# Performance work log

Hardware: AMD Instinct MI355X
Metric: run time of the kernel (lower is better)

The kernel has to match this reference:

```python
import jax, jax.numpy as jnp
import numpy as np

D_MODEL = 1024
EXPAND = 2
HEADDIM = 64
D_STATE = 64
CHUNK = 64
D_INNER = EXPAND * D_MODEL          # 2048
NHEADS = D_INNER // HEADDIM         # 32
D_MLP = int(2.5 * D_MODEL)          # 2560
BATCH = 2
SEQLEN = 4096
PROJ = 2 * D_INNER + 2 * NHEADS * D_STATE + NHEADS + NHEADS * (D_STATE // 2)


def rmsnorm(x, w, eps=1e-5):
    return x * jax.lax.rsqrt(jnp.mean(x * x, axis=-1, keepdims=True) + eps) * w


def apply_rope(x, angles):
    x1 = x[..., 0::2]
    x2 = x[..., 1::2]
    c = jnp.cos(angles)
    s = jnp.sin(angles)
    ev = c * x1 - s * x2
    od = s * x1 + c * x2
    return jnp.stack([ev, od], axis=-1).reshape(x.shape)


def segsum(x):
    # x: (b,h,c,l) -> (b,h,c,l,l); [i,j] = sum_{j<k<=i} x_k (no -inf mask, as in source)
    T = x.shape[-1]
    xx = jnp.broadcast_to(x[..., :, None], x.shape + (T,))
    mask = jnp.tril(jnp.ones((T, T), dtype=bool), -1)
    xx = jnp.where(mask, xx, 0.0)
    return jnp.cumsum(xx, axis=-2)


def ssd(x, A, B, C, chunk):
    # x: (b,s,h,p), A: (b,s,h), B/C: (b,s,h,n); s % chunk == 0
    b, s, h, p = x.shape
    n = B.shape[-1]
    c = s // chunk
    x_c = x.reshape(b, c, chunk, h, p).transpose(0, 1, 3, 2, 4)  # (b,c,h,l,p)
    B_c = B.reshape(b, c, chunk, h, n).transpose(0, 1, 3, 2, 4)  # (b,c,h,l,n)
    C_c = C.reshape(b, c, chunk, h, n).transpose(0, 1, 3, 2, 4)
    A_c = A.reshape(b, c, chunk, h).transpose(0, 1, 3, 2)        # (b,c,h,l)
    A_cum = jnp.cumsum(A_c, axis=-1)
    L = jnp.exp(segsum(A_c.transpose(0, 2, 1, 3))).transpose(0, 2, 1, 3, 4)  # (b,c,h,l,l)
    Bx = jnp.einsum('bchln,bchlp->bchpn', B_c, x_c)
    Y_diag = jnp.einsum('bchln,bchls,bchpn->bchlp', C_c, L, Bx)
    decay_states = jnp.exp(A_cum[..., -1:] - A_cum)
    states = jnp.einsum('bchln,bchl,bchlp->bchpn', B_c, decay_states, x_c)  # (b,c,h,p,n)
    decay_chunk = jnp.exp(A_cum[..., -1])  # (b,c,h)
    h0 = jnp.zeros_like(states[:, 0])

    def step(carry, inp):
        dec, st = inp  # dec: (b,h), st: (b,h,p,n)
        carry = carry * dec[:, :, None, None] + st
        return carry, carry

    _, hs = jax.lax.scan(step, h0, (decay_chunk.transpose(1, 0, 2),
                                    states.transpose(1, 0, 2, 3, 4)))
    final_states = hs.transpose(1, 0, 2, 3, 4)  # (b,c,h,p,n)
    Y_off = jnp.einsum('bchln,bchpn,bchl->bchlp', C_c, final_states, jnp.exp(A_cum))
    Y = (Y_diag + Y_off).transpose(0, 1, 3, 2, 4).reshape(b, s, h * p)
    return Y


def setup_inputs() -> dict:
    key = jax.random.key(0)
    ks = jax.random.split(key, 12)
    sc = 0.02
    return {
        'x': jax.random.normal(ks[0], (BATCH, SEQLEN, D_MODEL), jnp.float32),
        'norm1_w': jnp.ones((D_MODEL,), jnp.float32),
        'norm2_w': jnp.ones((D_MODEL,), jnp.float32),
        'W_in': sc * jax.random.normal(ks[1], (D_MODEL, PROJ), jnp.float32),
        'W_out': sc * jax.random.normal(ks[2], (D_INNER, D_MODEL), jnp.float32),
        'A_log': jax.random.uniform(ks[3], (NHEADS,), jnp.float32, -4.0, -1.0),
        'D_param': jnp.ones((NHEADS,), jnp.float32),
        'dt_bias': jax.random.uniform(ks[4], (NHEADS,), jnp.float32, 0.001, 0.1),
        'B_bias': jnp.ones((1, NHEADS, D_STATE), jnp.float32),
        'C_bias': jnp.ones((1, NHEADS, D_STATE), jnp.float32),
        'Bn_w': jnp.ones((D_STATE,), jnp.float32),
        'Cn_w': jnp.ones((D_STATE,), jnp.float32),
        'Wg': sc * jax.random.normal(ks[5], (D_MODEL, D_MLP), jnp.float32),
        'Wu': sc * jax.random.normal(ks[6], (D_MODEL, D_MLP), jnp.float32),
        'Wd': sc * jax.random.normal(ks[7], (D_MLP, D_MODEL), jnp.float32),
    }


def reference(x, norm1_w, norm2_w, W_in, W_out, A_log, D_param, dt_bias,
              B_bias, C_bias, Bn_w, Cn_w, Wg, Wu, Wd):
    b, s, _ = x.shape
    h = rmsnorm(x, norm1_w)
    proj = h @ W_in
    i = 0
    z = proj[..., i:i + D_INNER]; i += D_INNER
    x_ssm = proj[..., i:i + D_INNER]; i += D_INNER
    B = proj[..., i:i + NHEADS * D_STATE].reshape(b, s, NHEADS, D_STATE); i += NHEADS * D_STATE
    C = proj[..., i:i + NHEADS * D_STATE].reshape(b, s, NHEADS, D_STATE); i += NHEADS * D_STATE
    dt = proj[..., i:i + NHEADS]; i += NHEADS
    theta = proj[..., i:].reshape(b, s, NHEADS, D_STATE // 2)
    dt = jax.nn.softplus(dt + dt_bias)                 # (b,s,h)
    A = -jnp.exp(A_log) * dt
    alpha = jnp.exp(A)
    gamma = (alpha - 1.0) / (A + 1e-6) * 0.5 + 1.0
    B = rmsnorm(B, Bn_w) + B_bias
    C = rmsnorm(C, Cn_w) + C_bias
    cum_theta = jnp.cumsum(dt[..., None] * theta, axis=1)
    B = apply_rope(B, cum_theta)
    C = apply_rope(C, cum_theta)
    x_ssm = x_ssm.reshape(b, s, NHEADS, HEADDIM)
    y = ssd(x_ssm * gamma[..., None], A, B, C, CHUNK)
    skip = jnp.broadcast_to((D_param * x_ssm.sum(-1))[..., None], x_ssm.shape)
    y = y + skip.reshape(b, s, -1)
    y = y * (z * jax.nn.sigmoid(z))
    y = y @ W_out
    x = x + y
    h2 = rmsnorm(x, norm2_w)
    g = h2 @ Wg
    x = x + ((g * jax.nn.sigmoid(g)) * (h2 @ Wu)) @ Wd
    return x
```

## Files before the change

kernel.cpp:

```cpp
#include <hip/hip_runtime.h>
#include <cstdint>
#include <cmath>


typedef __bf16 bf16;
typedef __bf16 bf16x2 __attribute__((ext_vector_type(2)));
typedef __bf16 bf16x4 __attribute__((ext_vector_type(4)));
typedef __bf16 bf16x8 __attribute__((ext_vector_type(8)));
typedef float fx4 __attribute__((ext_vector_type(4)));

#define DEV __device__ __forceinline__

#define OFF_PROJ    0ull
#define OFF_HHI     134217728ull
#define OFF_HLO     150994944ull
#define OFF_WTIN    167772160ull
#define OFF_WTHI    184549376ull
#define OFF_WTLO    186908672ull
#define OFF_PROJT   189267968ull
#define OFF_BX      189267968ull
#define OFF_STATES  222822400ull
#define OFF_WTOUT   222822400ull
#define OFF_WTGU    227016704ull
#define OFF_WTD     237502464ull
#define OFF_ABUF    256376832ull
#define OFF_XSUM    257425408ull
#define OFF_ROWSUM  258473984ull
#define OFF_EXPA    260571136ull
#define OFF_DCHUNK  262668288ull
#define OFF_GAMMA   262684672ull
#define WS_NEEDED   263733248ull

#define OFF_GU      0ull
#define OFF_MBF     83886080ull

DEV void async_copy16(void* lds, const void* gptr) {
  __builtin_amdgcn_global_load_lds(
      (const __attribute__((address_space(1))) unsigned int*)(gptr),
      (__attribute__((address_space(3))) unsigned int*)(lds),
      16, 0, 0);
}

DEV float warp_sum64(float v) {
  #pragma unroll
  for (int o = 32; o; o >>= 1) v += __shfl_xor(v, o);
  return v;
}

DEV float red16(float v) {
  v += __shfl_xor(v, 1); v += __shfl_xor(v, 2);
  v += __shfl_xor(v, 4); v += __shfl_xor(v, 8);
  return v;
}

DEV float softplus_f(float x) { return x > 20.f ? x : log1pf(expf(x)); }
DEV float sigmoid_f(float x) { return 1.f / (1.f + expf(-x)); }

__global__ __launch_bounds__(256) void transpose_cast(
    const float* __restrict__ src, int ld, int col0,
    bf16* __restrict__ dst, int R, int C)
{
  __shared__ float tile[32][33];
  const int c0 = blockIdx.x * 32, r0 = blockIdx.y * 32;
  const int tx = threadIdx.x & 31, ty = threadIdx.x >> 5;
  #pragma unroll
  for (int ii = 0; ii < 4; ++ii) {
    int i = ty + ii * 8;
    int c = c0 + tx;
    tile[i][tx] = (c < C) ? src[(size_t)(r0 + i) * ld + col0 + c] : 0.f;
  }
  __syncthreads();
  #pragma unroll
  for (int ii = 0; ii < 4; ++ii) {
    int i = ty + ii * 8;
    dst[(size_t)(c0 + i) * R + r0 + tx] = (bf16)tile[tx][i];
  }
}

__global__ __launch_bounds__(256) void transpose_cast_hilo(
    const float* __restrict__ src, int ld, int col0,
    bf16* __restrict__ dhi, bf16* __restrict__ dlo, int R, int C)
{
  __shared__ float tile[32][33];
  const int c0 = blockIdx.x * 32, r0 = blockIdx.y * 32;
  const int tx = threadIdx.x & 31, ty = threadIdx.x >> 5;
  #pragma unroll
  for (int ii = 0; ii < 4; ++ii) {
    int i = ty + ii * 8;
    int c = c0 + tx;
    tile[i][tx] = (c < C) ? src[(size_t)(r0 + i) * ld + col0 + c] : 0.f;
  }
  __syncthreads();
  #pragma unroll
  for (int ii = 0; ii < 4; ++ii) {
    int i = ty + ii * 8;
    float v = tile[tx][i];
    bf16 hi = (bf16)v;
    size_t o = (size_t)(c0 + i) * R + r0 + tx;
    dhi[o] = hi;
    dlo[o] = (bf16)(v - (float)hi);
  }
}

__global__ __launch_bounds__(256) void rmsnorm_kernel(
    const float* __restrict__ x, const float* __restrict__ w,
    bf16* __restrict__ hi, bf16* __restrict__ lo)
{
  __shared__ float red[4];
  const size_t row = blockIdx.x;
  const int tid = threadIdx.x;
  float4 v = ((const float4*)(x + row * 1024))[tid];
  float ss = v.x * v.x + v.y * v.y + v.z * v.z + v.w * v.w;
  ss = warp_sum64(ss);
  if ((tid & 63) == 0) red[tid >> 6] = ss;
  __syncthreads();
  float tot = red[0] + red[1] + red[2] + red[3];
  float s = rsqrtf(tot * (1.f / 1024.f) + 1e-5f);
  float4 wv = ((const float4*)w)[tid];
  float h0 = v.x * s * wv.x, h1 = v.y * s * wv.y, h2 = v.z * s * wv.z, h3 = v.w * s * wv.w;
  bf16x4 hv = { (bf16)h0, (bf16)h1, (bf16)h2, (bf16)h3 };
  *(bf16x4*)(hi + row * 1024 + tid * 4) = hv;
  if (lo) {
    bf16x4 lv = { (bf16)(h0 - (float)hv[0]), (bf16)(h1 - (float)hv[1]),
                  (bf16)(h2 - (float)hv[2]), (bf16)(h3 - (float)hv[3]) };
    *(bf16x4*)(lo + row * 1024 + tid * 4) = lv;
  }
}

__global__ __launch_bounds__(256) void gemm_tail(
    const bf16* Ahi, const bf16* Alo, const bf16* Whi, const bf16* Wlo,
    float* Cout)
{
  __shared__ bf16 Ah[128 * 64], Al[128 * 64], Bh[128 * 64], Bl[128 * 64];
  const int tid = threadIdx.x, wid = tid >> 6, lane = tid & 63;
  const int m0 = blockIdx.y * 128, n0 = blockIdx.x * 128;
  const int wm = (wid & 1) * 64, wn = (wid >> 1) * 64;
  fx4 acc[4][4];
  #pragma unroll
  for (int i = 0; i < 4; ++i)
    #pragma unroll
    for (int j = 0; j < 4; ++j) { fx4 z = {0.f, 0.f, 0.f, 0.f}; acc[i][j] = z; }

  const int srow = wid * 32 + (lane >> 3);
  const int slot = lane & 7;

  for (int k0 = 0; k0 < 1024; k0 += 64) {
    __syncthreads();
    #pragma unroll
    for (int i = 0; i < 4; ++i) {
      int m = srow + i * 8;
      int cA = ((slot ^ (m & 7)) * 8);
      size_t ao = (size_t)(m0 + m) * 1024 + k0 + cA;
      async_copy16(&Ah[wid * 2048 + i * 512], Ahi + ao);
      async_copy16(&Al[wid * 2048 + i * 512], Alo + ao);
      int n = srow + i * 8;
      int cB = ((slot ^ (n & 7)) * 8);
      size_t bo = (size_t)(n0 + n) * 1024 + k0 + cB;
      async_copy16(&Bh[wid * 2048 + i * 512], Whi + bo);
      async_copy16(&Bl[wid * 2048 + i * 512], Wlo + bo);
    }
    __syncthreads();
    #pragma unroll
    for (int kk = 0; kk < 2; ++kk) {
      bf16x8 ah[4], al[4], bh[4], bl[4];
      #pragma unroll
      for (int i = 0; i < 4; ++i) {
        int mm = wm + i * 16 + (lane & 15);
        int sA = (kk * 4 + (lane >> 4)) ^ (mm & 7);
        ah[i] = *(const bf16x8*)&Ah[mm * 64 + sA * 8];
        al[i] = *(const bf16x8*)&Al[mm * 64 + sA * 8];
        int nn = wn + i * 16 + (lane & 15);
        int sB = (kk * 4 + (lane >> 4)) ^ (nn & 7);
        bh[i] = *(const bf16x8*)&Bh[nn * 64 + sB * 8];
        bl[i] = *(const bf16x8*)&Bl[nn * 64 + sB * 8];
      }
      #pragma unroll
      for (int i = 0; i < 4; ++i)
        #pragma unroll
        for (int j = 0; j < 4; ++j) {
          acc[i][j] = __builtin_amdgcn_mfma_f32_16x16x32_bf16(ah[i], bh[j], acc[i][j], 0, 0, 0);
          acc[i][j] = __builtin_amdgcn_mfma_f32_16x16x32_bf16(ah[i], bl[j], acc[i][j], 0, 0, 0);
          acc[i][j] = __builtin_amdgcn_mfma_f32_16x16x32_bf16(al[i], bh[j], acc[i][j], 0, 0, 0);
        }
    }
  }
  const int r0 = (lane >> 4) * 4, cc = lane & 15;
  #pragma unroll
  for (int i = 0; i < 4; ++i)
    #pragma unroll
    for (int j = 0; j < 4; ++j)
      #pragma unroll
      for (int r = 0; r < 4; ++r) {
        int m = m0 + wm + i * 16 + r0 + r;
        int n = n0 + wn + j * 16 + cc;
        Cout[(size_t)m * 1152 + n] = acc[i][j][r];
      }
}

__global__ __launch_bounds__(256) void dt_kernel(
    float* projT, const float* __restrict__ A_log, const float* __restrict__ dt_bias,
    float* __restrict__ a_buf, float* __restrict__ gamma_buf)
{
  const int idx = blockIdx.x * 256 + threadIdx.x;
  const int t = idx >> 5, h = idx & 31;
  float dtr = projT[(size_t)t * 1152 + h] + dt_bias[h];
  float dt = softplus_f(dtr);
  float a = -expf(A_log[h]) * dt;
  float alpha = expf(a);
  float gamma = (alpha - 1.f) / (a + 1e-6f) * 0.5f + 1.f;
  projT[(size_t)t * 1152 + h] = dt;
  a_buf[idx] = a;
  gamma_buf[idx] = gamma;
}

__global__ __launch_bounds__(512, 2) void gemm_proj256(
    const bf16* __restrict__ A, const bf16* __restrict__ B, bf16* __restrict__ Cout,
    const float* __restrict__ gamma_buf, float* __restrict__ xsum,
    const float* __restrict__ Bn_w, const float* __restrict__ Cn_w,
    const float* __restrict__ B_bias, const float* __restrict__ C_bias)
{
  __shared__ bf16 lds[65536];
  const int tid = threadIdx.x, wid = tid >> 6, lane = tid & 63;
  const int bid = blockIdx.x;
  const int swz = (bid & 7) * 128 + (bid >> 3);
  const int by = swz >> 5, bx = swz & 31;
  const int m0 = by * 256, n0 = bx * 256;
  const int wr = wid >> 2, wc = wid & 3;
  const int fl = lane & 15, fq = lane >> 4;
  const int rloc = wid * 8 + (lane >> 3);
  const int colSwz = ((lane & 7) ^ (lane >> 3)) * 8;

  fx4 acc[8][4];
  #pragma unroll
  for (int i = 0; i < 8; ++i)
    #pragma unroll
    for (int j = 0; j < 4; ++j) { fx4 z = {0.f, 0.f, 0.f, 0.f}; acc[i][j] = z; }

  const bf16* gA = A + (size_t)(m0 + rloc) * 1024 + colSwz;
  const bf16* gB = B + (size_t)(n0 + rloc) * 1024 + colSwz;

  auto STAGE = [&](int u, int h) {
    const bf16* s = (h < 2) ? gB : gA;
    s += (size_t)(h & 1) * 128 * 1024 + u * 64;
    bf16* d = &lds[((u & 1) * 4 + h) * 8192 + wid * 512];
    async_copy16(d, s);
    async_copy16(d + 4096, s + 64 * 1024);
  };

  STAGE(0, 0); STAGE(0, 1); STAGE(0, 2); STAGE(0, 3);
  STAGE(1, 0); STAGE(1, 1);
  asm volatile("s_waitcnt vmcnt(4)" ::: "memory");
  __builtin_amdgcn_s_barrier();

  const int NT = 16;
  bf16x8 bfrag[4][2];
  for (int t = 0; t < NT; ++t) {
    const int Bb = (t & 1) * 32768;
    const int Ab = Bb + 16384;
    #pragma unroll
    for (int p = 0; p < 4; ++p) {
      bf16x8 af[2][2];
      if (p == 0) {
        #pragma unroll
        for (int j = 0; j < 4; ++j) {
          int nn = wc * 64 + j * 16 + fl;
          #pragma unroll
          for (int kk = 0; kk < 2; ++kk) {
            int q = (kk * 4 + fq) ^ (nn & 7);
            bfrag[j][kk] = *(const bf16x8*)&lds[Bb + nn * 64 + q * 8];
          }
        }
      }
      #pragma unroll
      for (int ii = 0; ii < 2; ++ii) {
        int mm = wr * 128 + (p * 2 + ii) * 16 + fl;
        #pragma unroll
        for (int kk = 0; kk < 2; ++kk) {
          int q = (kk * 4 + fq) ^ (mm & 7);
          af[ii][kk] = *(const bf16x8*)&lds[Ab + mm * 64 + q * 8];
        }
      }
      {
        int H = 4 * t + 6 + p;
        if (H < 4 * NT) STAGE(H >> 2, H & 3);
      }
      if (p == 3) asm volatile("s_waitcnt vmcnt(4)" ::: "memory");
      __builtin_amdgcn_s_barrier();
      asm volatile("s_waitcnt lgkmcnt(0)" ::: "memory");
      __builtin_amdgcn_sched_barrier(0);
      __builtin_amdgcn_s_setprio(1);
      #pragma unroll
      for (int ii = 0; ii < 2; ++ii)
        #pragma unroll
        for (int j = 0; j < 4; ++j)
          #pragma unroll
          for (int kk = 0; kk < 2; ++kk)
            acc[p * 2 + ii][j] = __builtin_amdgcn_mfma_f32_16x16x32_bf16(
                af[ii][kk], bfrag[j][kk], acc[p * 2 + ii][j], 0, 0, 0);
      __builtin_amdgcn_s_setprio(0);
      __builtin_amdgcn_s_barrier();
    }
  }

  const int reg = bx >> 3;
  const int hh = ((n0 + wc * 64) & 2047) >> 6;
  const int mwb = m0 + wr * 128;
  const int nwb = n0 + wc * 64;
  if (reg == 0) {
    #pragma unroll
    for (int i = 0; i < 8; ++i)
      #pragma unroll
      for (int j = 0; j < 4; ++j)
        #pragma unroll
        for (int r = 0; r < 4; ++r) {
          int m = mwb + i * 16 + fq * 4 + r;
          int n = nwb + j * 16 + fl;
          Cout[(size_t)m * 8192 + n] = (bf16)acc[i][j][r];
        }
  } else if (reg == 1) {
    #pragma unroll
    for (int i = 0; i < 8; ++i)
      #pragma unroll
      for (int r = 0; r < 4; ++r) {
        float s = acc[i][0][r] + acc[i][1][r] + acc[i][2][r] + acc[i][3][r];
        s = red16(s);
        int m = mwb + i * 16 + fq * 4 + r;
        if (fl == 0) xsum[(size_t)m * 32 + hh] = s;
        float g = gamma_buf[(size_t)m * 32 + hh];
        #pragma unroll
        for (int j = 0; j < 4; ++j) {
          int n = nwb + j * 16 + fl;
          Cout[(size_t)m * 8192 + n] = (bf16)(acc[i][j][r] * g);
        }
      }
  } else {
    const float* w = (reg == 2) ? Bn_w : Cn_w;
    const float* bias = (reg == 2) ? B_bias : C_bias;
    #pragma unroll
    for (int i = 0; i < 8; ++i)
      #pragma unroll
      for (int r = 0; r < 4; ++r) {
        float ss = acc[i][0][r] * acc[i][0][r] + acc[i][1][r] * acc[i][1][r]
                 + acc[i][2][r] * acc[i][2][r] + acc[i][3][r] * acc[i][3][r];
        ss = red16(ss);
        float sc = rsqrtf(ss * (1.f / 64.f) + 1e-5f);
        int m = mwb + i * 16 + fq * 4 + r;
        #pragma unroll
        for (int j = 0; j < 4; ++j) {
          int c = j * 16 + fl;
          Cout[(size_t)m * 8192 + nwb + c] =
              (bf16)(acc[i][j][r] * sc * w[c] + bias[hh * 64 + c]);
        }
      }
  }
}

template <int MODE>
__global__ __launch_bounds__(512, 2) void gemm128x256(
    const bf16* __restrict__ A, const bf16* __restrict__ B, void* __restrict__ Cout,
    const float* __restrict__ resid, int NT, int lda, int ldc, int nbx)
{
  __shared__ bf16 lds[49152];
  const int tid = threadIdx.x, wid = tid >> 6, lane = tid & 63;
  const int cpx = gridDim.x >> 3;
  const int bid = blockIdx.x;
  const int swz = (bid & 7) * cpx + (bid >> 3);
  const int by = swz / nbx, bx = swz - by * nbx;
  const int m0 = by * 128, n0 = bx * 256;
  const int wr = wid >> 2, wc = wid & 3;
  const int fl = lane & 15, fq = lane >> 4;
  const int rloc = wid * 8 + (lane >> 3);
  const int colSwz = ((lane & 7) ^ (lane >> 3)) * 8;
  const int K = NT * 64;

  fx4 acc[4][4];
  #pragma unroll
  for (int i = 0; i < 4; ++i)
    #pragma unroll
    for (int j = 0; j < 4; ++j) { fx4 z = {0.f, 0.f, 0.f, 0.f}; acc[i][j] = z; }

  const bf16* gA = A + (size_t)(m0 + rloc) * lda + colSwz;
  const bf16* gB = B + (size_t)(n0 + rloc) * K + colSwz;

  auto STAGE = [&](int u, int h) {
    const bf16* s;
    size_t str;
    if (h < 2) { s = gB + (size_t)h * 128 * K; str = (size_t)K; }
    else       { s = gA;                       str = (size_t)lda; }
    s += u * 64;
    bf16* d = &lds[((u & 1) * 3 + h) * 8192 + wid * 512];
    async_copy16(d, s);
    async_copy16(d + 4096, s + 64 * str);
  };

  STAGE(0, 0); STAGE(0, 1); STAGE(0, 2);
  STAGE(1, 0); STAGE(1, 1);
  asm volatile("s_waitcnt vmcnt(4)" ::: "memory");
  __builtin_amdgcn_s_barrier();

  bf16x8 bfrag[4][2];
  for (int t = 0; t < NT; ++t) {
    const int base = (t & 1) * 24576;
    #pragma unroll
    for (int p = 0; p < 4; ++p) {
      bf16x8 af[2];
      if (p == 0) {
        #pragma unroll
        for (int j = 0; j < 4; ++j) {
          int nn = wc * 64 + j * 16 + fl;
          #pragma unroll
          for (int kk = 0; kk < 2; ++kk) {
            int q = (kk * 4 + fq) ^ (nn & 7);
            bfrag[j][kk] = *(const bf16x8*)&lds[base + (nn >> 7) * 8192 + (nn & 127) * 64 + q * 8];
          }
        }
      }
      {
        int mm = wr * 64 + p * 16 + fl;
        #pragma unroll
        for (int kk = 0; kk < 2; ++kk) {
          int q = (kk * 4 + fq) ^ (mm & 7);
          af[kk] = *(const bf16x8*)&lds[base + 2 * 8192 + mm * 64 + q * 8];
        }
      }
      if (p == 0)      { if (t + 1 < NT) STAGE(t + 1, 2); }
      else if (p == 1) { if (t + 2 < NT) STAGE(t + 2, 0); }
      else if (p == 2) { if (t + 2 < NT) STAGE(t + 2, 1); }
      if (p == 3) asm volatile("s_waitcnt vmcnt(4)" ::: "memory");
      __builtin_amdgcn_s_barrier();
      asm volatile("s_waitcnt lgkmcnt(0)" ::: "memory");
      __builtin_amdgcn_sched_barrier(0);
      __builtin_amdgcn_s_setprio(1);
      #pragma unroll
      for (int j = 0; j < 4; ++j)
        #pragma unroll
        for (int kk = 0; kk < 2; ++kk)
          acc[p][j] = __builtin_amdgcn_mfma_f32_16x16x32_bf16(
              af[kk], bfrag[j][kk], acc[p][j], 0, 0, 0);
      __builtin_amdgcn_s_setprio(0);
      __builtin_amdgcn_s_barrier();
    }
  }

  const int mwb = m0 + wr * 64;
  const int nwb = n0 + wc * 64;
  #pragma unroll
  for (int i = 0; i < 4; ++i)
    #pragma unroll
    for (int j = 0; j < 4; ++j)
      #pragma unroll
      for (int r = 0; r < 4; ++r) {
        int m = mwb + i * 16 + fq * 4 + r;
        int n = nwb + j * 16 + fl;
        size_t off = (size_t)m * ldc + n;
        float v = acc[i][j][r];
        if (MODE == 1) ((bf16*)Cout)[off] = (bf16)v;
        else ((float*)Cout)[off] = v + resid[off];
      }
}

__global__ __launch_bounds__(256) void chunk_sum_kernel(
    const float* __restrict__ projT, float* __restrict__ S)
{
  __shared__ float lds[8 * 288];
  const int blk = blockIdx.x;
  const int hq = blockIdx.y;
  const size_t row0 = (size_t)blk * 64;
  const int tid = threadIdx.x;
  float s = 0.f;
  #pragma unroll 1
  for (int batch = 0; batch < 8; ++batch) {
    __syncthreads();
    const float* src = projT + (row0 + batch * 8) * 1152;
    #pragma unroll
    for (int i = 0; i < 9; ++i) {
      int idx = i * 256 + tid;
      int r = idx / 288, col = idx - r * 288;
      int gcol = (col < 32) ? col : (32 + hq * 256 + (col - 32));
      lds[idx] = src[r * 1152 + gcol];
    }
    __syncthreads();
    int hl = tid >> 5, d = tid & 31;
    #pragma unroll
    for (int r = 0; r < 8; ++r)
      s += lds[r * 288 + hq * 8 + hl] * lds[r * 288 + 32 + hl * 32 + d];
  }
  S[(size_t)blk * 1024 + hq * 256 + tid] = s;
}

__global__ __launch_bounds__(256) void rope_kernel(
    bf16* proj, const float* __restrict__ projT, const float* __restrict__ S)
{
  __shared__ float angs[64 * 33], angc[64 * 33];
  const int blk = blockIdx.x;
  const int b = blk >> 11, c = (blk >> 5) & 63, h = blk & 31;
  const size_t t0 = (size_t)b * 4096 + c * 64;
  const int w = threadIdx.x >> 6, lane = threadIdx.x & 63;
  const float* tr = projT + (t0 + lane) * 1152;
  float dtv = tr[h];
  const float* thp = tr + 32 + h * 32 + w * 8;
  float4 th0 = *(const float4*)thp;
  float4 th1 = *(const float4*)(thp + 4);
  const float* Sp = S + (size_t)(b * 64 + lane) * 1024 + h * 32 + w * 8;
  float4 S0 = *(const float4*)Sp;
  float4 S1 = *(const float4*)(Sp + 4);
  float th[8] = { th0.x, th0.y, th0.z, th0.w, th1.x, th1.y, th1.z, th1.w };
  float Sv[8] = { S0.x, S0.y, S0.z, S0.w, S1.x, S1.y, S1.z, S1.w };
  #pragma unroll 1
  for (int j = 0; j < 8; ++j) {
    int d = w * 8 + j;
    float sv = (lane < c) ? Sv[j] : 0.f;
    float off = warp_sum64(sv);
    float v = dtv * th[j];
    #pragma unroll
    for (int o = 1; o < 64; o <<= 1) { float u = __shfl_up(v, o); if (lane >= o) v += u; }
    float ang = off + v;
    float sn, cs;
    sincosf(ang, &sn, &cs);
    angs[lane * 33 + d] = sn;
    angc[lane * 33 + d] = cs;
  }
  __syncthreads();
  const int tt = threadIdx.x >> 2, q = threadIdx.x & 3;
  const size_t base = (t0 + tt) * 8192 + 4096 + h * 64 + q * 16;
  #pragma unroll
  for (int m = 0; m < 2; ++m) {
    bf16* p = proj + base + m * 2048;
    bf16x8 v0 = *(const bf16x8*)(p);
    bf16x8 v1 = *(const bf16x8*)(p + 8);
    bf16x8 r0, r1;
    #pragma unroll
    for (int pp = 0; pp < 4; ++pp) {
      int d = q * 8 + pp;
      float e1 = (float)v0[2 * pp], e2 = (float)v0[2 * pp + 1];
      float sn = angs[tt * 33 + d], cs = angc[tt * 33 + d];
      r0[2 * pp]     = (bf16)(cs * e1 - sn * e2);
      r0[2 * pp + 1] = (bf16)(sn * e1 + cs * e2);
    }
    #pragma unroll
    for (int pp = 0; pp < 4; ++pp) {
      int d = q * 8 + 4 + pp;
      float e1 = (float)v1[2 * pp], e2 = (float)v1[2 * pp + 1];
      float sn = angs[tt * 33 + d], cs = angc[tt * 33 + d];
      r1[2 * pp]     = (bf16)(cs * e1 - sn * e2);
      r1[2 * pp + 1] = (bf16)(sn * e1 + cs * e2);
    }
    *(bf16x8*)(p) = r0;
    *(bf16x8*)(p + 8) = r1;
  }
}

__global__ __launch_bounds__(256) void ssd1_kernel(
    const bf16* __restrict__ proj, const float* __restrict__ a_buf,
    bf16* __restrict__ Bx, bf16* __restrict__ states,
    float* __restrict__ rowsum, float* __restrict__ expac, float* __restrict__ dchunk)
{
  __shared__ bf16 Xs[64 * 72], Bs[64 * 72];
  __shared__ float acum[64], dsv[64];
  const int blk = blockIdx.x;
  const int h = blk & 31;
  const size_t bs0 = ((size_t)(blk >> 5)) * 64;
  const int tid = threadIdx.x;
  const int l = tid >> 2, p0 = (tid & 3) * 16;
  {
    const bf16* xrow = proj + (bs0 + l) * 8192 + 2048 + h * 64 + p0;
    *(bf16x8*)&Xs[l * 72 + p0]     = ((const bf16x8*)xrow)[0];
    *(bf16x8*)&Xs[l * 72 + p0 + 8] = ((const bf16x8*)xrow)[1];
    const bf16* brow = proj + (bs0 + l) * 8192 + 4096 + h * 64 + p0;
    *(bf16x8*)&Bs[l * 72 + p0]     = ((const bf16x8*)brow)[0];
    *(bf16x8*)&Bs[l * 72 + p0 + 8] = ((const bf16x8*)brow)[1];
  }
  if (tid < 64) {
    float v = a_buf[(bs0 + tid) * 32 + h];
    #pragma unroll
    for (int o = 1; o < 64; o <<= 1) { float u = __shfl_up(v, o); if (tid >= o) v += u; }
    acum[tid] = v;
    float a63 = __shfl(v, 63);
    dsv[tid] = expf(a63 - v);
    expac[(size_t)blk * 64 + tid] = expf(v);
    if (tid == 63) dchunk[blk] = expf(v);
  }
  __syncthreads();
  {
    float al = acum[l];
    float rs = 0.f;
    for (int s = tid & 3; s <= l; s += 4) rs += expf(al - acum[s]);
    rs += __shfl_xor(rs, 1);
    rs += __shfl_xor(rs, 2);
    if ((tid & 3) == 0) rowsum[(size_t)blk * 64 + l] = rs + (float)(63 - l);
  }
  const int wv = tid >> 6, lane = tid & 63;
  const int mi = lane & 15, kq = lane >> 4;
  const int m0 = wv * 16;
  fx4 accB[4], accS[4];
  #pragma unroll
  for (int j4 = 0; j4 < 4; ++j4) { fx4 z = {0.f,0.f,0.f,0.f}; accB[j4] = z; accS[j4] = z; }
  #pragma unroll
  for (int kk = 0; kk < 2; ++kk) {
    const int lb = kk * 32 + kq * 8;
    bf16x8 aX, aXd;
    #pragma unroll
    for (int j = 0; j < 8; ++j) {
      bf16 xv = Xs[(lb + j) * 72 + m0 + mi];
      aX[j] = xv;
      aXd[j] = (bf16)((float)xv * dsv[lb + j]);
    }
    #pragma unroll
    for (int j4 = 0; j4 < 4; ++j4) {
      bf16x8 bB;
      #pragma unroll
      for (int j = 0; j < 8; ++j) bB[j] = Bs[(lb + j) * 72 + j4 * 16 + mi];
      accB[j4] = __builtin_amdgcn_mfma_f32_16x16x32_bf16(aX, bB, accB[j4], 0, 0, 0);
      accS[j4] = __builtin_amdgcn_mfma_f32_16x16x32_bf16(aXd, bB, accS[j4], 0, 0, 0);
    }
  }
  const size_t obase = (size_t)blk * 4096;
  #pragma unroll
  for (int j4 = 0; j4 < 4; ++j4) {
    #pragma unroll
    for (int r = 0; r < 4; ++r) {
      int p = m0 + kq * 4 + r;
      int n = j4 * 16 + mi;
      Bx[obase + p * 64 + n] = (bf16)accB[j4][r];
      states[obase + p * 64 + n] = (bf16)accS[j4][r];
    }
  }
}

__global__ __launch_bounds__(128) void ssd2_kernel(
    bf16* __restrict__ states, const float* __restrict__ dchunk)
{
  const int blk = blockIdx.x;
  const int b = blk >> 9, rest = blk & 511;
  const int h = rest >> 4, q = rest & 15;
  const int e0 = q * 256 + threadIdx.x * 2;
  float fs0 = 0.f, fs1 = 0.f;
  #pragma unroll 2
  for (int c = 0; c < 64; ++c) {
    size_t idx = ((size_t)(b * 2048 + c * 32 + h) * 4096) + e0;
    float dec = dchunk[b * 2048 + c * 32 + h];
    bf16x2 st = *(const bf16x2*)(states + idx);
    fs0 = fs0 * dec + (float)st[0];
    fs1 = fs1 * dec + (float)st[1];
    bf16x2 o = { (bf16)fs0, (bf16)fs1 };
    *(bf16x2*)(states + idx) = o;
  }
}

__global__ __launch_bounds__(256) void ssd3_kernel(
    bf16* proj, const bf16* __restrict__ Bx, const bf16* __restrict__ FS,
    const float* __restrict__ rowsum, const float* __restrict__ expac,
    const float* __restrict__ xsum, const float* __restrict__ D_param)
{
  __shared__ bf16 Cs[64 * 72], BxS[64 * 72], FSs[64 * 72];
  __shared__ float rs_s[64], ea_s[64], sk_s[64];
  const int blk = blockIdx.x;
  const int h = blk & 31;
  const size_t bs0 = ((size_t)(blk >> 5)) * 64;
  const int tid = threadIdx.x;
  const int l = tid >> 2, q0 = (tid & 3) * 16;
  {
    const bf16* crow = proj + (bs0 + l) * 8192 + 6144 + h * 64 + q0;
    *(bf16x8*)&Cs[l * 72 + q0]     = ((const bf16x8*)crow)[0];
    *(bf16x8*)&Cs[l * 72 + q0 + 8] = ((const bf16x8*)crow)[1];
    size_t mb = (size_t)blk * 4096 + l * 64 + q0;
    *(bf16x8*)&BxS[l * 72 + q0]     = ((const bf16x8*)(Bx + mb))[0];
    *(bf16x8*)&BxS[l * 72 + q0 + 8] = ((const bf16x8*)(Bx + mb))[1];
    *(bf16x8*)&FSs[l * 72 + q0]     = ((const bf16x8*)(FS + mb))[0];
    *(bf16x8*)&FSs[l * 72 + q0 + 8] = ((const bf16x8*)(FS + mb))[1];
  }
  if (tid < 64) {
    rs_s[tid] = rowsum[(size_t)blk * 64 + tid];
    ea_s[tid] = expac[(size_t)blk * 64 + tid];
    sk_s[tid] = D_param[h] * xsum[(bs0 + tid) * 32 + h];
  }
  __syncthreads();
  const int wv = tid >> 6, lane = tid & 63;
  const int mi = lane & 15, kq = lane >> 4;
  const int m0 = wv * 16;
  fx4 acc1[4], acc2[4];
  #pragma unroll
  for (int j4 = 0; j4 < 4; ++j4) { fx4 z = {0.f,0.f,0.f,0.f}; acc1[j4] = z; acc2[j4] = z; }
  #pragma unroll
  for (int kk = 0; kk < 2; ++kk) {
    bf16x8 aC = *(const bf16x8*)&Cs[(m0 + mi) * 72 + kk * 32 + kq * 8];
    #pragma unroll
    for (int j4 = 0; j4 < 4; ++j4) {
      bf16x8 bx = *(const bf16x8*)&BxS[(j4 * 16 + mi) * 72 + kk * 32 + kq * 8];
      bf16x8 fs = *(const bf16x8*)&FSs[(j4 * 16 + mi) * 72 + kk * 32 + kq * 8];
      acc1[j4] = __builtin_amdgcn_mfma_f32_16x16x32_bf16(aC, bx, acc1[j4], 0, 0, 0);
      acc2[j4] = __builtin_amdgcn_mfma_f32_16x16x32_bf16(aC, fs, acc2[j4], 0, 0, 0);
    }
  }
  #pragma unroll
  for (int j4 = 0; j4 < 4; ++j4) {
    #pragma unroll
    for (int r = 0; r < 4; ++r) {
      int li = m0 + kq * 4 + r;
      int p = j4 * 16 + mi;
      float y = rs_s[li] * acc1[j4][r] + ea_s[li] * acc2[j4][r] + sk_s[li];
      size_t zoff = (bs0 + li) * 8192 + h * 64 + p;
      float z = (float)proj[zoff];
      proj[zoff + 2048] = (bf16)(y * z * sigmoid_f(z));
    }
  }
}

__global__ __launch_bounds__(256) void silu_mul_kernel(
    const bf16* __restrict__ gu, bf16* __restrict__ m)
{
  const size_t row = blockIdx.y;
  const int col2 = blockIdx.x * 256 + threadIdx.x;
  const size_t gi = row * 5120 + col2 * 2;
  bf16x2 g = *(const bf16x2*)(gu + gi);
  bf16x2 u = *(const bf16x2*)(gu + gi + 2560);
  float g0 = (float)g[0], g1 = (float)g[1];
  float m0 = g0 * sigmoid_f(g0) * (float)u[0];
  float m1 = g1 * sigmoid_f(g1) * (float)u[1];
  bf16x2 mv = { (bf16)m0, (bf16)m1 };
  *(bf16x2*)(m + row * 2560 + col2 * 2) = mv;
}

extern "C" void kernel_launch(void* const* d_in, const int* in_sizes, int n_in,
                              void* d_out, int out_size, void* d_ws, size_t ws_size,
                              hipStream_t stream) {
  (void)in_sizes; (void)n_in; (void)out_size;
  if (ws_size < WS_NEEDED) return;
  const float* x       = (const float*)d_in[0];
  const float* n1w     = (const float*)d_in[1];
  const float* n2w     = (const float*)d_in[2];
  const float* W_in    = (const float*)d_in[3];
  const float* W_out   = (const float*)d_in[4];
  const float* A_log   = (const float*)d_in[5];
  const float* D_param = (const float*)d_in[6];
  const float* dt_bias = (const float*)d_in[7];
  const float* B_bias  = (const float*)d_in[8];
  const float* C_bias  = (const float*)d_in[9];
  const float* Bn_w    = (const float*)d_in[10];
  const float* Cn_w    = (const float*)d_in[11];
  const float* Wg      = (const float*)d_in[12];
  const float* Wu      = (const float*)d_in[13];
  const float* Wd      = (const float*)d_in[14];
  float* out = (float*)d_out;
  char* ws = (char*)d_ws;

  bf16*  proj   = (bf16*)(ws + OFF_PROJ);
  float* projT  = (float*)(ws + OFF_PROJT);
  bf16*  h_hi   = (bf16*)(ws + OFF_HHI);
  bf16*  h_lo   = (bf16*)(ws + OFF_HLO);
  bf16*  Wt_in  = (bf16*)(ws + OFF_WTIN);
  bf16*  Wt_hi  = (bf16*)(ws + OFF_WTHI);
  bf16*  Wt_lo  = (bf16*)(ws + OFF_WTLO);
  bf16*  Wt_out = (bf16*)(ws + OFF_WTOUT);
  bf16*  Wt_gu  = (bf16*)(ws + OFF_WTGU);
  bf16*  Wt_d   = (bf16*)(ws + OFF_WTD);
  bf16*  Bx     = (bf16*)(ws + OFF_BX);
  bf16*  states = (bf16*)(ws + OFF_STATES);
  float* a_buf  = (float*)(ws + OFF_ABUF);
  float* xsum_  = (float*)(ws + OFF_XSUM);
  float* rowsum = (float*)(ws + OFF_ROWSUM);
  float* expac  = (float*)(ws + OFF_EXPA);
  float* dchunk = (float*)(ws + OFF_DCHUNK);
  float* gamma_ = (float*)(ws + OFF_GAMMA);
  float* Ssum   = (float*)(ws + OFF_HLO);
  bf16*  ybf    = proj + 2048;
  bf16*  gubf   = (bf16*)(ws + OFF_GU);
  bf16*  mbf    = (bf16*)(ws + OFF_MBF);
  bf16*  h2bf   = h_hi;
  float* x2     = out;

  transpose_cast<<<dim3(256, 32), 256, 0, stream>>>(W_in, 9248, 0, Wt_in, 1024, 8192);
  transpose_cast_hilo<<<dim3(36, 32), 256, 0, stream>>>(W_in, 9248, 8192, Wt_hi, Wt_lo, 1024, 1056);

  rmsnorm_kernel<<<8192, 256, 0, stream>>>(x, n1w, h_hi, h_lo);

  gemm_tail<<<dim3(9, 64), 256, 0, stream>>>(h_hi, h_lo, Wt_hi, Wt_lo, projT);
  dt_kernel<<<1024, 256, 0, stream>>>(projT, A_log, dt_bias, a_buf, gamma_);
  gemm_proj256<<<dim3(1024), 512, 0, stream>>>(h_hi, Wt_in, proj, gamma_, xsum_,
                                               Bn_w, Cn_w, B_bias, C_bias);

  chunk_sum_kernel<<<dim3(128, 4), 256, 0, stream>>>(projT, Ssum);
  rope_kernel<<<4096, 256, 0, stream>>>(proj, projT, Ssum);

  ssd1_kernel<<<4096, 256, 0, stream>>>(proj, a_buf, Bx, states, rowsum, expac, dchunk);
  ssd2_kernel<<<1024, 128, 0, stream>>>(states, dchunk);
  ssd3_kernel<<<4096, 256, 0, stream>>>(proj, Bx, states, rowsum, expac, xsum_, D_param);

  transpose_cast<<<dim3(32, 64), 256, 0, stream>>>(W_out, 1024, 0, Wt_out, 2048, 1024);
  transpose_cast<<<dim3(80, 32), 256, 0, stream>>>(Wg, 2560, 0, Wt_gu, 1024, 2560);
  transpose_cast<<<dim3(80, 32), 256, 0, stream>>>(Wu, 2560, 0, Wt_gu + (size_t)2560 * 1024, 1024, 2560);
  transpose_cast<<<dim3(32, 80), 256, 0, stream>>>(Wd, 1024, 0, Wt_d, 2560, 1024);

  gemm128x256<2><<<dim3(256), 512, 0, stream>>>(ybf, Wt_out, x2, x, 32, 8192, 1024, 4);

  rmsnorm_kernel<<<8192, 256, 0, stream>>>(x2, n2w, h2bf, nullptr);
  gemm128x256<1><<<dim3(1280), 512, 0, stream>>>(h2bf, Wt_gu, gubf, nullptr, 16, 1024, 5120, 20);
  silu_mul_kernel<<<dim3(5, 8192), 256, 0, stream>>>(gubf, mbf);
  gemm128x256<2><<<dim3(256), 512, 0, stream>>>(mbf, Wt_d, out, x2, 40, 2560, 1024, 4);
}
```

Measured before the change: 783.0 us.

## Fuse gate/up GEMM with SiLU-multiply epilogue, drop intermediate gu buffer

Adds a dedicated GEMM in which half the waves compute the gate tile and half the up tile for the same 128x128 output region. The up results are exchanged through LDS so the epilogue writes silu(g)*u directly. This removes the 8192x5120 bf16 intermediate write and re-read and the separate elementwise kernel. It also changes the pipeline wait on the second-to-last iteration to vmcnt(0) in the existing GEMMs, which looks like a correctness fix for the tail prefetch and may add a small stall there.

Result: faster. 741.8 us (-5.3%).

```diff
diff --git a/kernel.cpp b/kernel.cpp
--- a/kernel.cpp
+++ b/kernel.cpp
@@ -31,7 +31,6 @@
 #define OFF_GAMMA   262684672ull
 #define WS_NEEDED   263733248ull
 
-#define OFF_GU      0ull
 #define OFF_MBF     83886080ull
 
 DEV void async_copy16(void* lds, const void* gptr) {
@@ -284,7 +283,10 @@
         int H = 4 * t + 6 + p;
         if (H < 4 * NT) STAGE(H >> 2, H & 3);
       }
-      if (p == 3) asm volatile("s_waitcnt vmcnt(4)" ::: "memory");
+      if (p == 3) {
+        if (t == NT - 2) asm volatile("s_waitcnt vmcnt(0)" ::: "memory");
+        else             asm volatile("s_waitcnt vmcnt(4)" ::: "memory");
+      }
       __builtin_amdgcn_s_barrier();
       asm volatile("s_waitcnt lgkmcnt(0)" ::: "memory");
       __builtin_amdgcn_sched_barrier(0);
@@ -426,7 +428,10 @@
       if (p == 0)      { if (t + 1 < NT) STAGE(t + 1, 2); }
       else if (p == 1) { if (t + 2 < NT) STAGE(t + 2, 0); }
       else if (p == 2) { if (t + 2 < NT) STAGE(t + 2, 1); }
-      if (p == 3) asm volatile("s_waitcnt vmcnt(4)" ::: "memory");
+      if (p == 3) {
+        if (t == NT - 2) asm volatile("s_waitcnt vmcnt(0)" ::: "memory");
+        else             asm volatile("s_waitcnt vmcnt(4)" ::: "memory");
+      }
       __builtin_amdgcn_s_barrier();
       asm volatile("s_waitcnt lgkmcnt(0)" ::: "memory");
       __builtin_amdgcn_sched_barrier(0);
@@ -457,6 +462,125 @@
         if (MODE == 1) ((bf16*)Cout)[off] = (bf16)v;
         else ((float*)Cout)[off] = v + resid[off];
       }
+}
+
+__global__ __launch_bounds__(512, 2) void gemm_gusilu(
+    const bf16* __restrict__ A, const bf16* __restrict__ B,
+    bf16* __restrict__ Mout, int nbx)
+{
+  __shared__ bf16 lds[49152];
+  const int tid = threadIdx.x, wid = tid >> 6, lane = tid & 63;
+  const int cpx = gridDim.x >> 3;
+  const int bid = blockIdx.x;
+  const int swz = (bid & 7) * cpx + (bid >> 3);
+  const int by = swz / nbx, bx = swz - by * nbx;
+  const int m0 = by * 128, n0 = bx * 128;
+  const int ws = wid >> 2;
+  const int wr = (wid >> 1) & 1, wc = wid & 1;
+  const int fl = lane & 15, fq = lane >> 4;
+  const int rloc = wid * 8 + (lane >> 3);
+  const int colSwz = ((lane & 7) ^ (lane >> 3)) * 8;
+  const int NT = 16, K = 1024;
+
+  fx4 acc[4][4];
+  #pragma unroll
+  for (int i = 0; i < 4; ++i)
+    #pragma unroll
+    for (int j = 0; j < 4; ++j) { fx4 z = {0.f, 0.f, 0.f, 0.f}; acc[i][j] = z; }
+
+  const bf16* gA  = A + (size_t)(m0 + rloc) * K + colSwz;
+  const bf16* gBg = B + (size_t)(n0 + rloc) * K + colSwz;
+  const bf16* gBu = B + (size_t)(2560 + n0 + rloc) * K + colSwz;
+
+  auto STAGE = [&](int u, int h) {
+    const bf16* s = (h == 0) ? gBg : (h == 1) ? gBu : gA;
+    s += u * 64;
+    bf16* d = &lds[((u & 1) * 3 + h) * 8192 + wid * 512];
+    async_copy16(d, s);
+    async_copy16(d + 4096, s + 64 * K);
+  };
+
+  STAGE(0, 0); STAGE(0, 1); STAGE(0, 2);
+  STAGE(1, 0); STAGE(1, 1);
+  asm volatile("s_waitcnt vmcnt(4)" ::: "memory");
+  __builtin_amdgcn_s_barrier();
+
+  bf16x8 bfrag[4][2];
+  for (int t = 0; t < NT; ++t) {
+    const int base = (t & 1) * 24576;
+    #pragma unroll
+    for (int p = 0; p < 4; ++p) {
+      bf16x8 af[2];
+      if (p == 0) {
+        #pragma unroll
+        for (int j = 0; j < 4; ++j) {
+          int nn = wc * 64 + j * 16 + fl;
+          #pragma unroll
+          for (int kk = 0; kk < 2; ++kk) {
+            int q = (kk * 4 + fq) ^ (nn & 7);
+            bfrag[j][kk] = *(const bf16x8*)&lds[base + ws * 8192 + nn * 64 + q * 8];
+          }
+        }
+      }
+      {
+        int mm = wr * 64 + p * 16 + fl;
+        #pragma unroll
+        for (int kk = 0; kk < 2; ++kk) {
+          int q = (kk * 4 + fq) ^ (mm & 7);
+          af[kk] = *(const bf16x8*)&lds[base + 2 * 8192 + mm * 64 + q * 8];
+        }
+      }
+      if (p == 0)      { if (t + 1 < NT) STAGE(t + 1, 2); }
+      else if (p == 1) { if (t + 2 < NT) STAGE(t + 2, 0); }
+      else if (p == 2) { if (t + 2 < NT) STAGE(t + 2, 1); }
+      if (p == 3) {
+        if (t == NT - 2) asm volatile("s_waitcnt vmcnt(0)" ::: "memory");
+        else             asm volatile("s_waitcnt vmcnt(4)" ::: "memory");
+      }
+      __builtin_amdgcn_s_barrier();
+      asm volatile("s_waitcnt lgkmcnt(0)" ::: "memory");
+      __builtin_amdgcn_sched_barrier(0);
+      __builtin_amdgcn_s_setprio(1);
+      #pragma unroll
+      for (int j = 0; j < 4; ++j)
+        #pragma unroll
+        for (int kk = 0; kk < 2; ++kk)
+          acc[p][j] = __builtin_amdgcn_mfma_f32_16x16x32_bf16(
+              af[kk], bfrag[j][kk], acc[p][j], 0, 0, 0);
+      __builtin_amdgcn_s_setprio(0);
+      __builtin_amdgcn_s_barrier();
+    }
+  }
+
+  float* uex = (float*)lds;
+  if (ws == 1) {
+    #pragma unroll
+    for (int i = 0; i < 4; ++i)
+      #pragma unroll
+      for (int j = 0; j < 4; ++j)
+        #pragma unroll
+        for (int r = 0; r < 4; ++r) {
+          int row = wr * 64 + i * 16 + fq * 4 + r;
+          int col = wc * 64 + j * 16 + fl;
+          uex[row * 132 + col] = acc[i][j][r];
+        }
+  }
+  __syncthreads();
+  if (ws == 0) {
+    #pragma unroll
+    for (int i = 0; i < 4; ++i)
+      #pragma unroll
+      for (int j = 0; j < 4; ++j)
+        #pragma unroll
+        for (int r = 0; r < 4; ++r) {
+          int row = wr * 64 + i * 16 + fq * 4 + r;
+          int col = wc * 64 + j * 16 + fl;
+          float g = acc[i][j][r];
+          float u = uex[row * 132 + col];
+          Mout[(size_t)(m0 + row) * 2560 + n0 + col] =
+              (bf16)(g * sigmoid_f(g) * u);
+        }
+  }
 }
 
 __global__ __launch_bounds__(256) void chunk_sum_kernel(
@@ -704,21 +828,6 @@
       proj[zoff + 2048] = (bf16)(y * z * sigmoid_f(z));
     }
   }
-}
-
-__global__ __launch_bounds__(256) void silu_mul_kernel(
-    const bf16* __restrict__ gu, bf16* __restrict__ m)
-{
-  const size_t row = blockIdx.y;
-  const int col2 = blockIdx.x * 256 + threadIdx.x;
-  const size_t gi = row * 5120 + col2 * 2;
-  bf16x2 g = *(const bf16x2*)(gu + gi);
-  bf16x2 u = *(const bf16x2*)(gu + gi + 2560);
-  float g0 = (float)g[0], g1 = (float)g[1];
-  float m0 = g0 * sigmoid_f(g0) * (float)u[0];
-  float m1 = g1 * sigmoid_f(g1) * (float)u[1];
-  bf16x2 mv = { (bf16)m0, (bf16)m1 };
-  *(bf16x2*)(m + row * 2560 + col2 * 2) = mv;
 }
 
 extern "C" void kernel_launch(void* const* d_in, const int* in_sizes, int n_in,
@@ -764,7 +873,6 @@
   float* gamma_ = (float*)(ws + OFF_GAMMA);
   float* Ssum   = (float*)(ws + OFF_HLO);
   bf16*  ybf    = proj + 2048;
-  bf16*  gubf   = (bf16*)(ws + OFF_GU);
   bf16*  mbf    = (bf16*)(ws + OFF_MBF);
   bf16*  h2bf   = h_hi;
   float* x2     = out;
@@ -794,7 +902,6 @@
   gemm128x256<2><<<dim3(256), 512, 0, stream>>>(ybf, Wt_out, x2, x, 32, 8192, 1024, 4);
 
   rmsnorm_kernel<<<8192, 256, 0, stream>>>(x2, n2w, h2bf, nullptr);
-  gemm128x256<1><<<dim3(1280), 512, 0, stream>>>(h2bf, Wt_gu, gubf, nullptr, 16, 1024, 5120, 20);
-  silu_mul_kernel<<<dim3(5, 8192), 256, 0, stream>>>(gubf, mbf);
+  gemm_gusilu<<<dim3(1280), 512, 0, stream>>>(h2bf, Wt_gu, mbf, 20);
   gemm128x256<2><<<dim3(256), 512, 0, stream>>>(mbf, Wt_d, out, x2, 40, 2560, 1024, 4);
 }
```
